# Kernel optimization log

Measured on AMD Instinct MI355X. Metric: run time of the kernel, lower is better.

Reference implementation:

```python
import jax, jax.numpy as jnp
import numpy as np

B, N, H, E = 64, 512, 32, 4
N_STEPS = 5
ANNO = 1


def setup_inputs() -> dict:
    key = jax.random.key(0)
    ks = jax.random.split(key, 20)
    sc_h = 1.0 / np.sqrt(H)
    sc_3h = 1.0 / np.sqrt(3 * H)
    sc_ha = 1.0 / np.sqrt(H + ANNO)
    inp = {
        "x": jax.random.normal(ks[0], (B, N, H), jnp.float32),
        "a": jax.random.uniform(ks[1], (B, N, ANNO), jnp.float32),
        "m": jax.random.uniform(ks[2], (B, N, 2 * N * E), jnp.float32),
        # fc_in / fc_out: hidden -> hidden*n_edge (torch Linear: W [out,in])
        "W_in": jax.random.normal(ks[3], (H * E, H), jnp.float32) * sc_h,
        "b_in": jax.random.normal(ks[4], (H * E,), jnp.float32) * sc_h,
        "W_out": jax.random.normal(ks[5], (H * E, H), jnp.float32) * sc_h,
        "b_out": jax.random.normal(ks[6], (H * E,), jnp.float32) * sc_h,
        # GRU-style gates: 3*hidden -> hidden
        "Wz": jax.random.normal(ks[7], (H, 3 * H), jnp.float32) * sc_3h,
        "bz": jax.random.normal(ks[8], (H,), jnp.float32) * sc_3h,
        "Wr": jax.random.normal(ks[9], (H, 3 * H), jnp.float32) * sc_3h,
        "br": jax.random.normal(ks[10], (H,), jnp.float32) * sc_3h,
        "Wt": jax.random.normal(ks[11], (H, 3 * H), jnp.float32) * sc_3h,
        "bt": jax.random.normal(ks[12], (H,), jnp.float32) * sc_3h,
        # output head (task_id not in {18,19}): fc1, fc2
        "W1": jax.random.normal(ks[13], (H, H + ANNO), jnp.float32) * sc_ha,
        "b1": jax.random.normal(ks[14], (H,), jnp.float32) * sc_ha,
        "W2": jax.random.normal(ks[15], (1, H), jnp.float32) * sc_h,
        "b2": jax.random.normal(ks[16], (1,), jnp.float32) * sc_h,
    }
    return inp


def _reorder(s):
    # [B, N, H*E] -> view(B,N,H,E) -> transpose(2,3) -> transpose(1,2) -> [B, E*N, H]
    return s.reshape(B, N, H, E).transpose(0, 3, 1, 2).reshape(B, E * N, H)


def reference(x, a, m, W_in, b_in, W_out, b_out, Wz, bz, Wr, br, Wt, bt, W1, b1, W2, b2):
    m_in = m[:, :, : N * E]   # [B, N, N*E]
    m_out = m[:, :, N * E :]  # [B, N, N*E]
    h = x
    for _ in range(N_STEPS):
        s_in = _reorder(h @ W_in.T + b_in)    # [B, E*N, H]
        s_out = _reorder(h @ W_out.T + b_out)  # [B, E*N, H]
        a_in = jnp.einsum("bnm,bmh->bnh", m_in, s_in)
        a_out = jnp.einsum("bnm,bmh->bnh", m_out, s_out)
        cat = jnp.concatenate([a_in, a_out, h], axis=-1)  # [B, N, 3H]
        z = jax.nn.sigmoid(cat @ Wz.T + bz)
        r = jax.nn.sigmoid(cat @ Wr.T + br)
        joint = jnp.concatenate([a_in, a_out, r * h], axis=-1)
        h_hat = jnp.tanh(joint @ Wt.T + bt)
        h = (1.0 - z) * h + z * h_hat
    out = jnp.tanh(jnp.concatenate([h, a], axis=-1) @ W1.T + b1)  # [B, N, H]
    out = (out @ W2.T + b2).sum(-1)  # [B, N]
    return out
```

## Files before the change

### kernel.cpp

```cpp
#include <hip/hip_runtime.h>
#include <hip/hip_fp16.h>
#include <math.h>

#define B_ 64
#define N_ 512
#define H_ 32
#define E_ 4
#define NSTEPS 5
#define KTOT 2048
#define KSPLIT 8
#define KCHUNK 256
#define ASLAB (B_*N_*H_)

typedef _Float16 half8 __attribute__((ext_vector_type(8)));
typedef float   f32x4 __attribute__((ext_vector_type(4)));

__global__ __launch_bounds__(256) void k_init_h(const float* __restrict__ x,
                                                float* __restrict__ h) {
    int i = blockIdx.x * blockDim.x + threadIdx.x;
    ((f32x4*)h)[i] = ((const f32x4*)x)[i];
}

__global__ __launch_bounds__(256) void k_s(const float* __restrict__ hstate,
                                           const float* __restrict__ W_in,
                                           const float* __restrict__ b_in,
                                           const float* __restrict__ W_out,
                                           const float* __restrict__ b_out,
                                           _Float16* __restrict__ sT_in_hi,
                                           _Float16* __restrict__ sT_in_lo,
                                           _Float16* __restrict__ sT_out_hi,
                                           _Float16* __restrict__ sT_out_lo) {
    int b  = blockIdx.x >> 3;
    int n0 = (blockIdx.x & 7) * 64;
    int lane = threadIdx.x & 63;
    int w = __builtin_amdgcn_readfirstlane((int)(threadIdx.x >> 6));
    int n = n0 + lane;

    const float* hrow = hstate + ((size_t)b * N_ + n) * H_;
    f32x4 hv[8];
#pragma unroll
    for (int c = 0; c < 8; c++) hv[c] = ((const f32x4*)hrow)[c];

#pragma unroll 4
    for (int o = 0; o < 32; o++) {
        int he = w * 32 + o;
        const f32x4* wr = (const f32x4*)(W_in + (size_t)he * H_);
        float acc = b_in[he];
#pragma unroll
        for (int c = 0; c < 8; c++) {
            f32x4 wv = wr[c];
            acc += hv[c][0]*wv[0] + hv[c][1]*wv[1] + hv[c][2]*wv[2] + hv[c][3]*wv[3];
        }
        int hh = he >> 2, e = he & 3;
        size_t idx = ((size_t)b * H_ + hh) * KTOT + e * N_ + n;
        _Float16 hi = (_Float16)acc;
        sT_in_hi[idx] = hi;
        sT_in_lo[idx] = (_Float16)(acc - (float)hi);
    }
#pragma unroll 4
    for (int o = 0; o < 32; o++) {
        int he = w * 32 + o;
        const f32x4* wr = (const f32x4*)(W_out + (size_t)he * H_);
        float acc = b_out[he];
#pragma unroll
        for (int c = 0; c < 8; c++) {
            f32x4 wv = wr[c];
            acc += hv[c][0]*wv[0] + hv[c][1]*wv[1] + hv[c][2]*wv[2] + hv[c][3]*wv[3];
        }
        int hh = he >> 2, e = he & 3;
        size_t idx = ((size_t)b * H_ + hh) * KTOT + e * N_ + n;
        _Float16 hi = (_Float16)acc;
        sT_out_hi[idx] = hi;
        sT_out_lo[idx] = (_Float16)(acc - (float)hi);
    }
}

__global__ __launch_bounds__(256) void k_einsum_l(const float* __restrict__ m,
                                                  const _Float16* __restrict__ sT_in_hi,
                                                  const _Float16* __restrict__ sT_in_lo,
                                                  const _Float16* __restrict__ sT_out_hi,
                                                  const _Float16* __restrict__ sT_out_lo,
                                                  float* __restrict__ apart) {
    int split = blockIdx.x;
    int b     = blockIdx.y;
    int dir   = blockIdx.z;
    int tid   = threadIdx.x;
    int w     = tid >> 6;
    int lane  = tid & 63;
    int l15   = lane & 15;
    int quad  = lane >> 4;

    __shared__ __align__(16) char smem[32768];

    const _Float16* sHi = (dir ? sT_out_hi : sT_in_hi)
                          + (size_t)b * H_ * KTOT + split * KCHUNK;
    const _Float16* sLo = (dir ? sT_out_lo : sT_in_lo)
                          + (size_t)b * H_ * KTOT + split * KCHUNK;

    for (int i = tid; i < 2048; i += 256) {
        int plane = i >> 10, row = (i >> 5) & 31, c16 = i & 31;
        const _Float16* src = (plane ? sLo : sHi) + (size_t)row * KTOT + c16 * 8;
        half8 v = *(const half8*)src;
        int byte = plane * 16384 + row * 512 + ((c16 * 16) ^ ((row & 7) << 4));
        *(half8*)(smem + byte) = v;
    }
    __syncthreads();

    float* aout = apart + (size_t)(dir * KSPLIT + split) * ASLAB;
    int swz0 = (l15 & 7) << 4;

#pragma unroll 2
    for (int pass = 0; pass < 8; pass++) {
        int n0 = pass * 64;
        const float* mrow = m + ((size_t)b * N_ + n0 + w * 16 + l15) * (2 * KTOT)
                              + (size_t)dir * KTOT + split * KCHUNK;

        f32x4 acc0 = {0.f,0.f,0.f,0.f}, acc1 = {0.f,0.f,0.f,0.f};

#pragma unroll 2
        for (int it = 0; it < 8; it++) {
            int ko = it * 32 + quad * 8;
            f32x4 a0 = *(const f32x4*)(mrow + ko);
            f32x4 a1 = *(const f32x4*)(mrow + ko + 4);

            int kb = it * 64 + quad * 16;
            int o0 = l15 * 512        + (kb ^ swz0);
            int o1 = (l15 + 16) * 512 + (kb ^ swz0);
            half8 Bhi0 = *(const half8*)(smem + o0);
            half8 Bhi1 = *(const half8*)(smem + o1);
            half8 Blo0 = *(const half8*)(smem + 16384 + o0);
            half8 Blo1 = *(const half8*)(smem + 16384 + o1);

            half8 Ahi, Alo;
#pragma unroll
            for (int j = 0; j < 4; j++) {
                float v0 = a0[j], v1 = a1[j];
                _Float16 h0 = (_Float16)v0, h1 = (_Float16)v1;
                Ahi[j]     = h0;
                Ahi[j + 4] = h1;
                Alo[j]     = (_Float16)(v0 - (float)h0);
                Alo[j + 4] = (_Float16)(v1 - (float)h1);
            }
            acc0 = __builtin_amdgcn_mfma_f32_16x16x32_f16(Ahi, Bhi0, acc0, 0, 0, 0);
            acc1 = __builtin_amdgcn_mfma_f32_16x16x32_f16(Ahi, Bhi1, acc1, 0, 0, 0);
            acc0 = __builtin_amdgcn_mfma_f32_16x16x32_f16(Ahi, Blo0, acc0, 0, 0, 0);
            acc1 = __builtin_amdgcn_mfma_f32_16x16x32_f16(Ahi, Blo1, acc1, 0, 0, 0);
            acc0 = __builtin_amdgcn_mfma_f32_16x16x32_f16(Alo, Bhi0, acc0, 0, 0, 0);
            acc1 = __builtin_amdgcn_mfma_f32_16x16x32_f16(Alo, Bhi1, acc1, 0, 0, 0);
        }

#pragma unroll
        for (int r = 0; r < 4; r++) {
            size_t rr = (size_t)b * N_ + (n0 + w * 16 + quad * 4 + r);
            aout[rr * H_ + l15]      = acc0[r];
            aout[rr * H_ + 16 + l15] = acc1[r];
        }
    }
}

__global__ __launch_bounds__(256) void k_gate(const float* __restrict__ apart,
                                              float* __restrict__ hstate,
                                              const float* __restrict__ Wz,
                                              const float* __restrict__ bz,
                                              const float* __restrict__ Wr,
                                              const float* __restrict__ br,
                                              const float* __restrict__ Wt,
                                              const float* __restrict__ bt) {
    __shared__ float cat[8][96];
    __shared__ float rh[8][32];
    int base = blockIdx.x * 8;
    int t = threadIdx.x;

    for (int idx = t; idx < 768; idx += 256) {
        int r = idx / 96, c = idx - r * 96;
        size_t row = (size_t)(base + r);
        float v;
        if (c < 64) {
            int d = c >> 5;
            const float* p = apart + (size_t)d * KSPLIT * ASLAB + row * 32 + (c & 31);
            v = p[0];
#pragma unroll
            for (int s2 = 1; s2 < KSPLIT; s2++) v += p[(size_t)s2 * ASLAB];
        } else {
            v = hstate[row * 32 + (c - 64)];
        }
        cat[r][c] = v;
    }
    __syncthreads();

    int r = t >> 5, i = t & 31;
    float az = bz[i], ar = br[i];
    const f32x4* wzr = (const f32x4*)(Wz + (size_t)i * 96);
    const f32x4* wrr = (const f32x4*)(Wr + (size_t)i * 96);
    const f32x4* crow = (const f32x4*)cat[r];
#pragma unroll
    for (int kc = 0; kc < 24; kc++) {
        f32x4 cv = crow[kc];
        f32x4 wz = wzr[kc];
        f32x4 wr = wrr[kc];
        az += cv[0]*wz[0] + cv[1]*wz[1] + cv[2]*wz[2] + cv[3]*wz[3];
        ar += cv[0]*wr[0] + cv[1]*wr[1] + cv[2]*wr[2] + cv[3]*wr[3];
    }
    float z  = 1.f / (1.f + __expf(-az));
    float rg = 1.f / (1.f + __expf(-ar));
    float hold = cat[r][64 + i];
    rh[r][i] = rg * hold;
    __syncthreads();

    float at = bt[i];
    const f32x4* wtr = (const f32x4*)(Wt + (size_t)i * 96);
#pragma unroll
    for (int kc = 0; kc < 16; kc++) {
        f32x4 cv = crow[kc];
        f32x4 wt = wtr[kc];
        at += cv[0]*wt[0] + cv[1]*wt[1] + cv[2]*wt[2] + cv[3]*wt[3];
    }
    const f32x4* rrow = (const f32x4*)rh[r];
#pragma unroll
    for (int kc = 0; kc < 8; kc++) {
        f32x4 cv = rrow[kc];
        f32x4 wt = wtr[16 + kc];
        at += cv[0]*wt[0] + cv[1]*wt[1] + cv[2]*wt[2] + cv[3]*wt[3];
    }
    float hh = tanhf(at);
    hstate[(size_t)(base + r) * 32 + i] = (1.f - z) * hold + z * hh;
}

__global__ __launch_bounds__(256) void k_final(const float* __restrict__ hstate,
                                               const float* __restrict__ a,
                                               const float* __restrict__ W1,
                                               const float* __restrict__ b1,
                                               const float* __restrict__ W2,
                                               const float* __restrict__ b2,
                                               float* __restrict__ out) {
    __shared__ float hl[8][32];
    __shared__ float as[8];
    int base = blockIdx.x * 8;
    int t = threadIdx.x;
    {
        int r = t >> 5, c = t & 31;
        hl[r][c] = hstate[(size_t)(base + r) * 32 + c];
        if (t < 8) as[t] = a[base + t];
    }
    __syncthreads();
    int r = t >> 5, j = t & 31;
    float acc = b1[j];
    const float* w1r = W1 + (size_t)j * 33;
#pragma unroll
    for (int i2 = 0; i2 < 32; i2++) acc += hl[r][i2] * w1r[i2];
    acc += as[r] * w1r[32];
    float o = tanhf(acc) * W2[j];
#pragma unroll
    for (int off = 16; off; off >>= 1) o += __shfl_xor(o, off, 32);
    if (j == 0) out[base + r] = o + b2[0];
}

extern "C" void kernel_launch(void* const* d_in, const int* in_sizes, int n_in,
                              void* d_out, int out_size, void* d_ws, size_t ws_size,
                              hipStream_t stream) {
    const float* x     = (const float*)d_in[0];
    const float* a     = (const float*)d_in[1];
    const float* m     = (const float*)d_in[2];
    const float* W_in  = (const float*)d_in[3];
    const float* b_in  = (const float*)d_in[4];
    const float* W_out = (const float*)d_in[5];
    const float* b_out = (const float*)d_in[6];
    const float* Wz    = (const float*)d_in[7];
    const float* bz    = (const float*)d_in[8];
    const float* Wr    = (const float*)d_in[9];
    const float* br    = (const float*)d_in[10];
    const float* Wt    = (const float*)d_in[11];
    const float* bt    = (const float*)d_in[12];
    const float* W1    = (const float*)d_in[13];
    const float* b1    = (const float*)d_in[14];
    const float* W2    = (const float*)d_in[15];
    const float* b2    = (const float*)d_in[16];
    float* out = (float*)d_out;

    char* ws = (char*)d_ws;
    float*    h         = (float*)(ws);
    float*    apart     = (float*)(ws + ((size_t)4  << 20));
    _Float16* sT_in_hi  = (_Float16*)(ws + ((size_t)68 << 20));
    _Float16* sT_in_lo  = (_Float16*)(ws + ((size_t)76 << 20));
    _Float16* sT_out_hi = (_Float16*)(ws + ((size_t)84 << 20));
    _Float16* sT_out_lo = (_Float16*)(ws + ((size_t)92 << 20));

    k_init_h<<<1024, 256, 0, stream>>>(x, h);
    for (int s = 0; s < NSTEPS; s++) {
        k_s<<<512, 256, 0, stream>>>(h, W_in, b_in, W_out, b_out,
                                     sT_in_hi, sT_in_lo, sT_out_hi, sT_out_lo);
        k_einsum_l<<<dim3(KSPLIT, 64, 2), 256, 0, stream>>>(m, sT_in_hi, sT_in_lo,
                                                            sT_out_hi, sT_out_lo,
                                                            apart);
        k_gate<<<4096, 256, 0, stream>>>(apart, h, Wz, bz, Wr, br, Wt, bt);
    }
    k_final<<<4096, 256, 0, stream>>>(h, a, W1, b1, W2, b2, out);
}
```

Measured before the change: 2.401 ms.

## Reassociate edge-linear through adjacency: pack m once, GEMM m·h, apply weights in gate

Instead of projecting h through W_in/W_out and then multiplying by m each step, the per-edge adjacency blocks are multiplied by h directly, and the edge weights are applied afterwards in the gate kernel. The bias term is handled through precomputed row sums of m. The adjacency matrix is split once into fp16 hi/lo parts in a blocked layout, so each step streams fp16 instead of re-reading and converting fp32 m. This adds a 512MB packed buffer and one pack pass. The new path is gated on workspace size and falls back to the old path if the workspace is too small.

Measured after the change: 2.692 ms. 12.1% more time.

```diff
diff --git a/kernel.cpp b/kernel.cpp
--- a/kernel.cpp
+++ b/kernel.cpp
@@ -19,6 +19,231 @@
                                                 float* __restrict__ h) {
     int i = blockIdx.x * blockDim.x + threadIdx.x;
     ((f32x4*)h)[i] = ((const f32x4*)x)[i];
+}
+
+
+__global__ __launch_bounds__(256) void k_pack(const float* __restrict__ m,
+                                              _Float16* __restrict__ pHi,
+                                              _Float16* __restrict__ pLo,
+                                              float* __restrict__ msum) {
+    __shared__ __align__(16) char lds[65536];
+    int p = blockIdx.x;
+    int g = blockIdx.y;
+    int b = g >> 3, dir = (g >> 2) & 1, e = g & 3;
+    int tid = threadIdx.x;
+    int w = tid >> 6, lane = tid & 63, l15 = lane & 15, quad = lane >> 4;
+
+    const float* mbase = m + ((size_t)(b * N_ + p * 64 + w * 16) * (2 * KTOT))
+                           + dir * KTOT + e * 512;
+    char* myl = lds + w * 16384;
+    size_t obase = ((((size_t)g * 8 + p) * 4 + w) * 16) * 512;
+    float s_acc = 0.f;
+
+    for (int half = 0; half < 2; half++) {
+        __syncthreads();
+        for (int r = 0; r < 16; r++) {
+            f32x4 v = *(const f32x4*)(mbase + (size_t)r * (2 * KTOT)
+                                      + half * 256 + lane * 4);
+            int byte = r * 1024 + ((lane * 16) ^ ((r & 7) << 4));
+            *(f32x4*)(myl + byte) = v;
+        }
+        __syncthreads();
+        for (int it = 0; it < 8; it++) {
+            int kf = it * 32 + quad * 8;
+            int swz = (l15 & 7) << 4;
+            int byte0 = l15 * 1024 + ((kf * 4) ^ swz);
+            int byte1 = l15 * 1024 + (((kf + 4) * 4) ^ swz);
+            f32x4 v0 = *(const f32x4*)(myl + byte0);
+            f32x4 v1 = *(const f32x4*)(myl + byte1);
+            half8 hi, lo;
+#pragma unroll
+            for (int j = 0; j < 4; j++) {
+                float v = v0[j];
+                _Float16 hh = (_Float16)v;
+                hi[j] = hh; lo[j] = (_Float16)(v - (float)hh);
+                s_acc += v;
+            }
+#pragma unroll
+            for (int j = 0; j < 4; j++) {
+                float v = v1[j];
+                _Float16 hh = (_Float16)v;
+                hi[j + 4] = hh; lo[j + 4] = (_Float16)(v - (float)hh);
+                s_acc += v;
+            }
+            size_t o = obase + (size_t)(half * 8 + it) * 512 + lane * 8;
+            *(half8*)(pHi + o) = hi;
+            *(half8*)(pLo + o) = lo;
+        }
+    }
+    s_acc += __shfl_xor(s_acc, 16);
+    s_acc += __shfl_xor(s_acc, 32);
+    if (quad == 0) {
+        int n = p * 64 + w * 16 + l15;
+        msum[(((size_t)b * N_ + n) * 2 + dir) * 4 + e] = s_acc;
+    }
+}
+
+__global__ __launch_bounds__(256) void k_gemm(const float* __restrict__ h,
+                                              const _Float16* __restrict__ pHi,
+                                              const _Float16* __restrict__ pLo,
+                                              float* __restrict__ G) {
+    int eh  = blockIdx.x;
+    int e   = eh & 3, kh = eh >> 2;
+    int b   = blockIdx.y;
+    int dir = blockIdx.z;
+    int g   = (b * 2 + dir) * 4 + e;
+    int tid = threadIdx.x;
+    int w = tid >> 6, lane = tid & 63, l15 = lane & 15, quad = lane >> 4;
+
+    __shared__ __align__(16) char hT[32768];
+
+    for (int i = tid; i < 2048; i += 256) {
+        int np = i >> 3, cg = i & 7;
+        f32x4 v = *(const f32x4*)(h + ((size_t)b * N_ + kh * 256 + np) * H_ + cg * 4);
+#pragma unroll
+        for (int j = 0; j < 4; j++) {
+            int c = cg * 4 + j;
+            float vv = v[j];
+            _Float16 hh = (_Float16)vv;
+            _Float16 ll = (_Float16)(vv - (float)hh);
+            int base = c * 512 + ((np * 2) ^ ((c & 7) << 4));
+            *(_Float16*)(hT + base) = hh;
+            *(_Float16*)(hT + 16384 + base) = ll;
+        }
+    }
+    __syncthreads();
+
+    float* Gout = G + ((size_t)g * 2 + kh) * 16384;
+    int swz = (l15 & 7) << 4;
+
+    for (int p = 0; p < 8; p++) {
+        size_t abase = ((((size_t)g * 8 + p) * 4 + w) * 16 + kh * 8) * 512
+                       + (size_t)lane * 8;
+        f32x4 acc0 = {0.f,0.f,0.f,0.f}, acc1 = {0.f,0.f,0.f,0.f};
+
+#pragma unroll 2
+        for (int it = 0; it < 8; it++) {
+            half8 Ahi = *(const half8*)(pHi + abase + (size_t)it * 512);
+            half8 Alo = *(const half8*)(pLo + abase + (size_t)it * 512);
+
+            int kb = (it * 32 + quad * 8) * 2;
+            int o0 = l15 * 512        + (kb ^ swz);
+            int o1 = (l15 + 16) * 512 + (kb ^ swz);
+            half8 Bhi0 = *(const half8*)(hT + o0);
+            half8 Bhi1 = *(const half8*)(hT + o1);
+            half8 Blo0 = *(const half8*)(hT + 16384 + o0);
+            half8 Blo1 = *(const half8*)(hT + 16384 + o1);
+
+            acc0 = __builtin_amdgcn_mfma_f32_16x16x32_f16(Ahi, Bhi0, acc0, 0, 0, 0);
+            acc1 = __builtin_amdgcn_mfma_f32_16x16x32_f16(Ahi, Bhi1, acc1, 0, 0, 0);
+            acc0 = __builtin_amdgcn_mfma_f32_16x16x32_f16(Ahi, Blo0, acc0, 0, 0, 0);
+            acc1 = __builtin_amdgcn_mfma_f32_16x16x32_f16(Ahi, Blo1, acc1, 0, 0, 0);
+            acc0 = __builtin_amdgcn_mfma_f32_16x16x32_f16(Alo, Bhi0, acc0, 0, 0, 0);
+            acc1 = __builtin_amdgcn_mfma_f32_16x16x32_f16(Alo, Bhi1, acc1, 0, 0, 0);
+        }
+
+#pragma unroll
+        for (int r = 0; r < 4; r++) {
+            int rr = p * 64 + w * 16 + quad * 4 + r;
+            Gout[(size_t)rr * 32 + l15]      = acc0[r];
+            Gout[(size_t)rr * 32 + 16 + l15] = acc1[r];
+        }
+    }
+}
+
+__global__ __launch_bounds__(256) void k_gate2(const float* __restrict__ G,
+                                               const float* __restrict__ msum,
+                                               float* __restrict__ hstate,
+                                               const float* __restrict__ W_in,
+                                               const float* __restrict__ b_in,
+                                               const float* __restrict__ W_out,
+                                               const float* __restrict__ b_out,
+                                               const float* __restrict__ Wz,
+                                               const float* __restrict__ bz,
+                                               const float* __restrict__ Wr,
+                                               const float* __restrict__ br,
+                                               const float* __restrict__ Wt,
+                                               const float* __restrict__ bt) {
+    __shared__ float Gs[8][256];
+    __shared__ float cat[8][96];
+    __shared__ float rh[8][32];
+    int base = blockIdx.x * 8;
+    int t = threadIdx.x;
+    int b = base >> 9;
+
+    for (int i = t; i < 2048; i += 256) {
+        int r = i >> 8, c = i & 255;
+        int dir = c >> 7, e = (c >> 5) & 3, hp = c & 31;
+        int n = (base + r) & 511;
+        size_t gg = ((size_t)(b * 2 + dir) * 4 + e) * 2;
+        size_t off = (size_t)n * 32 + hp;
+        Gs[r][c] = G[gg * 16384 + off] + G[(gg + 1) * 16384 + off];
+    }
+    __syncthreads();
+
+    int r = t >> 5, i = t & 31;
+    {
+        int n = (base + r) & 511;
+        const float* ms = msum + ((size_t)b * N_ + n) * 8;
+        float a0 = 0.f, a1 = 0.f;
+#pragma unroll
+        for (int e = 0; e < 4; e++) {
+            int he = i * 4 + e;
+            a0 += ms[e]     * b_in[he];
+            a1 += ms[4 + e] * b_out[he];
+            const f32x4* wi = (const f32x4*)(W_in  + (size_t)he * 32);
+            const f32x4* wo = (const f32x4*)(W_out + (size_t)he * 32);
+            const f32x4* g0 = (const f32x4*)&Gs[r][e * 32];
+            const f32x4* g1 = (const f32x4*)&Gs[r][128 + e * 32];
+#pragma unroll
+            for (int q = 0; q < 8; q++) {
+                f32x4 gv0 = g0[q], wv0 = wi[q];
+                f32x4 gv1 = g1[q], wv1 = wo[q];
+                a0 += gv0[0]*wv0[0] + gv0[1]*wv0[1] + gv0[2]*wv0[2] + gv0[3]*wv0[3];
+                a1 += gv1[0]*wv1[0] + gv1[1]*wv1[1] + gv1[2]*wv1[2] + gv1[3]*wv1[3];
+            }
+        }
+        cat[r][i]      = a0;
+        cat[r][32 + i] = a1;
+        cat[r][64 + i] = hstate[(size_t)(base + r) * 32 + i];
+    }
+    __syncthreads();
+
+    float az = bz[i], ar = br[i];
+    const f32x4* wzr = (const f32x4*)(Wz + (size_t)i * 96);
+    const f32x4* wrr = (const f32x4*)(Wr + (size_t)i * 96);
+    const f32x4* crow = (const f32x4*)cat[r];
+#pragma unroll
+    for (int kc = 0; kc < 24; kc++) {
+        f32x4 cv = crow[kc];
+        f32x4 wz = wzr[kc];
+        f32x4 wr = wrr[kc];
+        az += cv[0]*wz[0] + cv[1]*wz[1] + cv[2]*wz[2] + cv[3]*wz[3];
+        ar += cv[0]*wr[0] + cv[1]*wr[1] + cv[2]*wr[2] + cv[3]*wr[3];
+    }
+    float z  = 1.f / (1.f + __expf(-az));
+    float rg = 1.f / (1.f + __expf(-ar));
+    float hold = cat[r][64 + i];
+    rh[r][i] = rg * hold;
+    __syncthreads();
+
+    float at = bt[i];
+    const f32x4* wtr = (const f32x4*)(Wt + (size_t)i * 96);
+#pragma unroll
+    for (int kc = 0; kc < 16; kc++) {
+        f32x4 cv = crow[kc];
+        f32x4 wt = wtr[kc];
+        at += cv[0]*wt[0] + cv[1]*wt[1] + cv[2]*wt[2] + cv[3]*wt[3];
+    }
+    const f32x4* rrow = (const f32x4*)rh[r];
+#pragma unroll
+    for (int kc = 0; kc < 8; kc++) {
+        f32x4 cv = rrow[kc];
+        f32x4 wt = wtr[16 + kc];
+        at += cv[0]*wt[0] + cv[1]*wt[1] + cv[2]*wt[2] + cv[3]*wt[3];
+    }
+    float hh = tanhf(at);
+    hstate[(size_t)(base + r) * 32 + i] = (1.f - z) * hold + z * hh;
 }
 
 __global__ __launch_bounds__(256) void k_s(const float* __restrict__ hstate,
@@ -278,21 +503,38 @@
     float* out = (float*)d_out;
 
     char* ws = (char*)d_ws;
-    float*    h         = (float*)(ws);
-    float*    apart     = (float*)(ws + ((size_t)4  << 20));
-    _Float16* sT_in_hi  = (_Float16*)(ws + ((size_t)68 << 20));
-    _Float16* sT_in_lo  = (_Float16*)(ws + ((size_t)76 << 20));
-    _Float16* sT_out_hi = (_Float16*)(ws + ((size_t)84 << 20));
-    _Float16* sT_out_lo = (_Float16*)(ws + ((size_t)92 << 20));
+    float* h = (float*)(ws);
+
+    const int use_new = (ws_size >= ((size_t)592 << 20));
 
     k_init_h<<<1024, 256, 0, stream>>>(x, h);
-    for (int s = 0; s < NSTEPS; s++) {
-        k_s<<<512, 256, 0, stream>>>(h, W_in, b_in, W_out, b_out,
-                                     sT_in_hi, sT_in_lo, sT_out_hi, sT_out_lo);
-        k_einsum_l<<<dim3(KSPLIT, 64, 2), 256, 0, stream>>>(m, sT_in_hi, sT_in_lo,
-                                                            sT_out_hi, sT_out_lo,
-                                                            apart);
-        k_gate<<<4096, 256, 0, stream>>>(apart, h, Wz, bz, Wr, br, Wt, bt);
+
+    if (use_new) {
+        float*    G      = (float*)(ws + ((size_t)4  << 20));
+        float*    msum   = (float*)(ws + ((size_t)68 << 20));
+        _Float16* pHi    = (_Float16*)(ws + ((size_t)80  << 20));
+        _Float16* pLo    = (_Float16*)(ws + ((size_t)336 << 20));
+
+        k_pack<<<dim3(8, 512), 256, 0, stream>>>(m, pHi, pLo, msum);
+        for (int s = 0; s < NSTEPS; s++) {
+            k_gemm<<<dim3(8, 64, 2), 256, 0, stream>>>(h, pHi, pLo, G);
+            k_gate2<<<4096, 256, 0, stream>>>(G, msum, h, W_in, b_in, W_out, b_out,
+                                              Wz, bz, Wr, br, Wt, bt);
+        }
+    } else {
+        float*    apart     = (float*)(ws + ((size_t)4  << 20));
+        _Float16* sT_in_hi  = (_Float16*)(ws + ((size_t)68 << 20));
+        _Float16* sT_in_lo  = (_Float16*)(ws + ((size_t)76 << 20));
+        _Float16* sT_out_hi = (_Float16*)(ws + ((size_t)84 << 20));
+        _Float16* sT_out_lo = (_Float16*)(ws + ((size_t)92 << 20));
+        for (int s = 0; s < NSTEPS; s++) {
+            k_s<<<512, 256, 0, stream>>>(h, W_in, b_in, W_out, b_out,
+                                         sT_in_hi, sT_in_lo, sT_out_hi, sT_out_lo);
+            k_einsum_l<<<dim3(KSPLIT, 64, 2), 256, 0, stream>>>(m, sT_in_hi, sT_in_lo,
+                                                                sT_out_hi, sT_out_lo,
+                                                                apart);
+            k_gate<<<4096, 256, 0, stream>>>(apart, h, Wz, bz, Wr, br, Wt, bt);
+        }
     }
     k_final<<<4096, 256, 0, stream>>>(h, a, W1, b1, W2, b2, out);
 }
```

## Fuse all GGNN steps into one cooperative persistent kernel with reassociated einsum

Applied to the files above, without the earlier changes.

Replaces the per-step chain of s-projection, einsum and gate kernels with a single cooperative kernel that loops over steps, using grid.sync between them. The einsum is reassociated as (m @ h) @ W. The edge-projection bias is added through row sums of m, which are computed once in step 0. h is staged in LDS as split fp16 hi/lo for MFMA. This removes the intermediate s tensors, their global round trips and the extra kernel launches. The cost is a single 1024-thread block per CU, a heavy LDS footprint and grid-wide barriers, with the old path kept as a fallback.

New measurement: 2.863 ms. +19.2%, slower.

```diff
diff --git a/kernel.cpp b/kernel.cpp
--- a/kernel.cpp
+++ b/kernel.cpp
@@ -1,6 +1,9 @@
 #include <hip/hip_runtime.h>
+#include <hip/hip_cooperative_groups.h>
 #include <hip/hip_fp16.h>
 #include <math.h>
+
+namespace cg = cooperative_groups;
 
 #define B_ 64
 #define N_ 512
@@ -14,6 +17,193 @@
 
 typedef _Float16 half8 __attribute__((ext_vector_type(8)));
 typedef float   f32x4 __attribute__((ext_vector_type(4)));
+
+struct P2 {
+    const float *x, *a, *m;
+    const float *W_in, *b_in, *W_out, *b_out;
+    const float *Wz, *bz, *Wr, *br, *Wt, *bt;
+    const float *W1, *b1, *W2, *b2;
+    float *out;
+    float *h;
+};
+
+__global__ __launch_bounds__(1024) void k_steps(P2 p) {
+    cg::grid_group grid = cg::this_grid();
+    const int bid = blockIdx.x;
+    const int b  = bid >> 2, nb = bid & 3;
+    const int R0 = nb * 128;
+    const int tid = threadIdx.x;
+    const int lane = tid & 63;
+    const int wv   = tid >> 6;
+    const int l15  = lane & 15, quad = lane >> 4;
+    const int rowtile = wv >> 1, coltile = wv & 1;
+    const int ig = tid & 31, rg = tid >> 5;
+
+    __shared__ __align__(16) char hT[2][32768];
+    __shared__ float Gs[128][32];
+    __shared__ float aLds[128][64];
+    __shared__ float msumL[128][8];
+    __shared__ float rhL[32][32];
+    __shared__ float hOld[128][32];
+
+    const size_t hbase = (size_t)b * N_ * H_;
+
+    for (int s = 0; s < NSTEPS; s++) {
+        if (s > 0) grid.sync();
+        const float* hsrc = (s == 0 ? p.x : p.h) + hbase;
+
+        for (int i = tid; i < 4096; i += 1024) {
+            int np = i >> 3, c4 = i & 7;
+            f32x4 v = *(const f32x4*)(hsrc + (size_t)np * H_ + c4 * 4);
+#pragma unroll
+            for (int j = 0; j < 4; j++) {
+                int c = c4 * 4 + j;
+                float vv = v[j];
+                _Float16 hh = (_Float16)vv;
+                _Float16 ll = (_Float16)(vv - (float)hh);
+                int off = c * 1024 + ((np * 2) ^ ((c & 7) << 4));
+                *(_Float16*)(&hT[0][0] + off) = hh;
+                *(_Float16*)(&hT[1][0] + off) = ll;
+            }
+        }
+        for (int i = tid; i < 4096; i += 1024)
+            hOld[i >> 5][i & 31] = hsrc[(size_t)(R0 + (i >> 5)) * H_ + (i & 31)];
+        __syncthreads();
+
+        float aReg[2][4];
+#pragma unroll
+        for (int d2 = 0; d2 < 2; d2++)
+#pragma unroll
+            for (int rx = 0; rx < 4; rx++) aReg[d2][rx] = 0.f;
+
+#pragma unroll
+        for (int dir = 0; dir < 2; dir++) {
+            const float* Wf = dir ? p.W_out : p.W_in;
+            const float* bf = dir ? p.b_out : p.b_in;
+            for (int e = 0; e < 4; e++) {
+                const float* mrow = p.m
+                    + ((size_t)(b * N_ + R0 + rowtile * 16 + l15)) * (2 * KTOT)
+                    + (size_t)dir * KTOT + e * 512;
+                const int brow = coltile * 16 + l15;
+                const int bswz = (brow & 7) << 4;
+                const int boff = brow * 1024;
+                f32x4 acc = {0.f, 0.f, 0.f, 0.f};
+                float sac = 0.f;
+#pragma unroll 4
+                for (int kk = 0; kk < 16; kk++) {
+                    int k0 = kk * 32 + quad * 8;
+                    f32x4 a0 = *(const f32x4*)(mrow + k0);
+                    f32x4 a1 = *(const f32x4*)(mrow + k0 + 4);
+                    half8 Ahi, Alo;
+#pragma unroll
+                    for (int j = 0; j < 4; j++) {
+                        float v0 = a0[j], v1 = a1[j];
+                        _Float16 h0 = (_Float16)v0, h1 = (_Float16)v1;
+                        Ahi[j]     = h0;
+                        Ahi[j + 4] = h1;
+                        Alo[j]     = (_Float16)(v0 - (float)h0);
+                        Alo[j + 4] = (_Float16)(v1 - (float)h1);
+                    }
+                    if (s == 0)
+                        sac += a0[0]+a0[1]+a0[2]+a0[3]+a1[0]+a1[1]+a1[2]+a1[3];
+                    int off = boff + ((k0 * 2) ^ bswz);
+                    half8 Bhi = *(const half8*)(&hT[0][0] + off);
+                    half8 Blo = *(const half8*)(&hT[1][0] + off);
+                    acc = __builtin_amdgcn_mfma_f32_16x16x32_f16(Ahi, Bhi, acc, 0, 0, 0);
+                    acc = __builtin_amdgcn_mfma_f32_16x16x32_f16(Ahi, Blo, acc, 0, 0, 0);
+                    acc = __builtin_amdgcn_mfma_f32_16x16x32_f16(Alo, Bhi, acc, 0, 0, 0);
+                }
+                if (s == 0 && coltile == 0) {
+                    sac += __shfl_xor(sac, 16);
+                    sac += __shfl_xor(sac, 32);
+                    if (quad == 0) msumL[rowtile * 16 + l15][dir * 4 + e] = sac;
+                }
+#pragma unroll
+                for (int r = 0; r < 4; r++)
+                    Gs[rowtile * 16 + quad * 4 + r][coltile * 16 + l15] = acc[r];
+                __syncthreads();
+
+                const float* wrow = Wf + (size_t)(ig * 4 + e) * 32;
+                float msb = bf[ig * 4 + e];
+#pragma unroll
+                for (int rx = 0; rx < 4; rx++) {
+                    int row = rg + rx * 32;
+                    const f32x4* g  = (const f32x4*)Gs[row];
+                    const f32x4* wq = (const f32x4*)wrow;
+                    float t = msumL[row][dir * 4 + e] * msb;
+#pragma unroll
+                    for (int q = 0; q < 8; q++) {
+                        f32x4 gv = g[q], wvv = wq[q];
+                        t += gv[0]*wvv[0] + gv[1]*wvv[1] + gv[2]*wvv[2] + gv[3]*wvv[3];
+                    }
+                    aReg[dir][rx] += t;
+                }
+                __syncthreads();
+            }
+#pragma unroll
+            for (int rx = 0; rx < 4; rx++)
+                aLds[rg + rx * 32][dir * 32 + ig] = aReg[dir][rx];
+        }
+        __syncthreads();
+
+        for (int ps = 0; ps < 4; ps++) {
+            int row = ps * 32 + rg;
+            float az = p.bz[ig], ar = p.br[ig];
+            const f32x4* wz = (const f32x4*)(p.Wz + (size_t)ig * 96);
+            const f32x4* wr = (const f32x4*)(p.Wr + (size_t)ig * 96);
+            const f32x4* ca = (const f32x4*)aLds[row];
+            const f32x4* ch = (const f32x4*)hOld[row];
+#pragma unroll
+            for (int kc = 0; kc < 16; kc++) {
+                f32x4 cv = ca[kc], z1 = wz[kc], r1 = wr[kc];
+                az += cv[0]*z1[0] + cv[1]*z1[1] + cv[2]*z1[2] + cv[3]*z1[3];
+                ar += cv[0]*r1[0] + cv[1]*r1[1] + cv[2]*r1[2] + cv[3]*r1[3];
+            }
+#pragma unroll
+            for (int kc = 0; kc < 8; kc++) {
+                f32x4 cv = ch[kc], z1 = wz[16 + kc], r1 = wr[16 + kc];
+                az += cv[0]*z1[0] + cv[1]*z1[1] + cv[2]*z1[2] + cv[3]*z1[3];
+                ar += cv[0]*r1[0] + cv[1]*r1[1] + cv[2]*r1[2] + cv[3]*r1[3];
+            }
+            float zg    = 1.f / (1.f + __expf(-az));
+            float rgate = 1.f / (1.f + __expf(-ar));
+            float hold  = hOld[row][ig];
+            rhL[rg][ig] = rgate * hold;
+            __syncthreads();
+            float at = p.bt[ig];
+            const f32x4* wt = (const f32x4*)(p.Wt + (size_t)ig * 96);
+#pragma unroll
+            for (int kc = 0; kc < 16; kc++) {
+                f32x4 cv = ca[kc], t1 = wt[kc];
+                at += cv[0]*t1[0] + cv[1]*t1[1] + cv[2]*t1[2] + cv[3]*t1[3];
+            }
+            const f32x4* rr = (const f32x4*)rhL[rg];
+#pragma unroll
+            for (int kc = 0; kc < 8; kc++) {
+                f32x4 cv = rr[kc], t1 = wt[16 + kc];
+                at += cv[0]*t1[0] + cv[1]*t1[1] + cv[2]*t1[2] + cv[3]*t1[3];
+            }
+            float hh2  = tanhf(at);
+            float hnew = (1.f - zg) * hold + zg * hh2;
+            p.h[hbase + (size_t)(R0 + row) * H_ + ig] = hnew;
+            hOld[row][ig] = hnew;
+            __syncthreads();
+        }
+    }
+
+    for (int ps = 0; ps < 4; ps++) {
+        int row = ps * 32 + rg;
+        float acc = p.b1[ig];
+        const float* w1r = p.W1 + (size_t)ig * 33;
+#pragma unroll
+        for (int i2 = 0; i2 < 32; i2++) acc += hOld[row][i2] * w1r[i2];
+        acc += p.a[(size_t)b * N_ + R0 + row] * w1r[32];
+        float o = tanhf(acc) * p.W2[ig];
+#pragma unroll
+        for (int off = 16; off; off >>= 1) o += __shfl_xor(o, off, 32);
+        if (ig == 0) p.out[(size_t)b * N_ + R0 + row] = o + p.b2[0];
+    }
+}
 
 __global__ __launch_bounds__(256) void k_init_h(const float* __restrict__ x,
                                                 float* __restrict__ h) {
@@ -278,21 +468,45 @@
     float* out = (float*)d_out;
 
     char* ws = (char*)d_ws;
-    float*    h         = (float*)(ws);
-    float*    apart     = (float*)(ws + ((size_t)4  << 20));
-    _Float16* sT_in_hi  = (_Float16*)(ws + ((size_t)68 << 20));
-    _Float16* sT_in_lo  = (_Float16*)(ws + ((size_t)76 << 20));
-    _Float16* sT_out_hi = (_Float16*)(ws + ((size_t)84 << 20));
-    _Float16* sT_out_lo = (_Float16*)(ws + ((size_t)92 << 20));
-
-    k_init_h<<<1024, 256, 0, stream>>>(x, h);
-    for (int s = 0; s < NSTEPS; s++) {
-        k_s<<<512, 256, 0, stream>>>(h, W_in, b_in, W_out, b_out,
-                                     sT_in_hi, sT_in_lo, sT_out_hi, sT_out_lo);
-        k_einsum_l<<<dim3(KSPLIT, 64, 2), 256, 0, stream>>>(m, sT_in_hi, sT_in_lo,
-                                                            sT_out_hi, sT_out_lo,
-                                                            apart);
-        k_gate<<<4096, 256, 0, stream>>>(apart, h, Wz, bz, Wr, br, Wt, bt);
-    }
-    k_final<<<4096, 256, 0, stream>>>(h, a, W1, b1, W2, b2, out);
-}
+    float* h = (float*)(ws);
+
+    P2 prm;
+    prm.x = x; prm.a = a; prm.m = m;
+    prm.W_in = W_in; prm.b_in = b_in; prm.W_out = W_out; prm.b_out = b_out;
+    prm.Wz = Wz; prm.bz = bz; prm.Wr = Wr; prm.br = br; prm.Wt = Wt; prm.bt = bt;
+    prm.W1 = W1; prm.b1 = b1; prm.W2 = W2; prm.b2 = b2;
+    prm.out = out; prm.h = h;
+
+    static int coop_ok = -1;
+    if (coop_ok < 0) {
+        int v = 0;
+        hipDeviceGetAttribute(&v, hipDeviceAttributeCooperativeLaunch, 0);
+        coop_ok = v;
+    }
+
+    hipError_t err = hipErrorUnknown;
+    if (coop_ok) {
+        void* args[] = { (void*)&prm };
+        err = hipLaunchCooperativeKernel((const void*)k_steps,
+                                         dim3(256), dim3(1024), args, 0, stream);
+    }
+    if (err != hipSuccess) {
+        (void)hipGetLastError();
+        float*    apart     = (float*)(ws + ((size_t)4  << 20));
+        _Float16* sT_in_hi  = (_Float16*)(ws + ((size_t)68 << 20));
+        _Float16* sT_in_lo  = (_Float16*)(ws + ((size_t)76 << 20));
+        _Float16* sT_out_hi = (_Float16*)(ws + ((size_t)84 << 20));
+        _Float16* sT_out_lo = (_Float16*)(ws + ((size_t)92 << 20));
+
+        k_init_h<<<1024, 256, 0, stream>>>(x, h);
+        for (int s = 0; s < NSTEPS; s++) {
+            k_s<<<512, 256, 0, stream>>>(h, W_in, b_in, W_out, b_out,
+                                         sT_in_hi, sT_in_lo, sT_out_hi, sT_out_lo);
+            k_einsum_l<<<dim3(KSPLIT, 64, 2), 256, 0, stream>>>(m, sT_in_hi, sT_in_lo,
+                                                                sT_out_hi, sT_out_lo,
+                                                                apart);
+            k_gate<<<4096, 256, 0, stream>>>(apart, h, Wz, bz, Wr, br, Wt, bt);
+        }
+        k_final<<<4096, 256, 0, stream>>>(h, a, W1, b1, W2, b2, out);
+    }
+}
```
